# Kernel tuning notes

Hardware: AMD Instinct MI355X
Metric: run time of the kernel (lower is better)

## Reference

```python
import jax, jax.numpy as jnp
import numpy as np

N = 4096
FEAT = 5
H = 128
L = 3
K = 4
HD = H // K  # 32


def setup_inputs() -> dict:
    key = jax.random.key(0)
    ks = jax.random.split(key, 24)
    node_features = jax.random.normal(ks[0], (N, FEAT), dtype=jnp.float32)
    u = jax.random.uniform(ks[1], (N, N), dtype=jnp.float32)
    adj = jnp.where(u < 0.01, u, 0.0)
    adj = adj / (adj.sum(axis=1, keepdims=True) + 1e-8)  # row-normalised
    mask = jax.random.randint(ks[2], (N,), 0, 2).astype(bool)
    s = 0.05
    return {
        'node_features': node_features,
        'adj': adj,
        'mask': mask,
        'Wi': jax.random.normal(ks[3], (FEAT, H), jnp.float32) * s,
        'bi': jnp.zeros((H,), jnp.float32),
        'gat_W': jax.random.normal(ks[4], (L, K, H, HD), jnp.float32) * s,
        'gat_a': jax.random.normal(ks[5], (L, K, 2 * HD), jnp.float32) * s,
        'ln_g': jnp.ones((L, H), jnp.float32),
        'ln_b': jnp.zeros((L, H), jnp.float32),
        'pW1': jax.random.normal(ks[6], (H, H // 2), jnp.float32) * s,
        'pb1': jnp.zeros((H // 2,), jnp.float32),
        'pW2': jax.random.normal(ks[7], (H // 2, 1), jnp.float32) * s,
        'pb2': jnp.zeros((1,), jnp.float32),
        'poolW': jax.random.normal(ks[8], (H, H), jnp.float32) * s,
        'poolb': jnp.zeros((H,), jnp.float32),
        'poolv': jax.random.normal(ks[9], (H,), jnp.float32) * s,
        'vW1': jax.random.normal(ks[10], (H, H // 2), jnp.float32) * s,
        'vb1': jnp.zeros((H // 2,), jnp.float32),
        'vW2': jax.random.normal(ks[11], (H // 2, 1), jnp.float32) * s,
        'vb2': jnp.zeros((1,), jnp.float32),
    }


def _layernorm(x, g, b, eps=1e-5):
    mu = x.mean(-1, keepdims=True)
    var = ((x - mu) ** 2).mean(-1, keepdims=True)
    return (x - mu) / jnp.sqrt(var + eps) * g + b


def reference(node_features, adj, mask, Wi, bi, gat_W, gat_a, ln_g, ln_b,
              pW1, pb1, pW2, pb2, poolW, poolb, poolv, vW1, vb1, vW2, vb2):
    n = node_features.shape[0]
    x = jax.nn.relu(node_features @ Wi + bi)  # (N, H)
    edge_mask = (adj > 0) | jnp.eye(n, dtype=bool)  # (N, N) incl self-loops
    n_layers = gat_W.shape[0]
    for l in range(n_layers):
        Wx = jnp.einsum('nd,kdh->knh', x, gat_W[l])  # (K, N, hd)
        a_src = jnp.einsum('knh,kh->kn', Wx, gat_a[l][:, :HD])  # (K, N)
        a_dst = jnp.einsum('knh,kh->kn', Wx, gat_a[l][:, HD:])  # (K, N)
        e = jax.nn.leaky_relu(a_src[:, :, None] + a_dst[:, None, :], 0.2)  # (K,N,N)
        e = jnp.where(edge_mask[None], e, -jnp.inf)
        alpha = jax.nn.softmax(e, axis=-1)  # softmax over neighbours j
        h = jax.nn.elu(jnp.einsum('kij,kjh->kih', alpha, Wx))  # (K, N, hd)
        out = jnp.transpose(h, (1, 0, 2)).reshape(n, -1)  # concat heads -> (N, H)
        out = out + x  # residual (Identity: in_dim == out_dim)
        x = _layernorm(out, ln_g[l], ln_b[l])
    # policy head
    logits = (jax.nn.relu(x @ pW1 + pb1) @ pW2 + pb2).squeeze(-1)  # (N,)
    logits = jnp.where(mask, logits, -jnp.inf)
    # attention pooling restricted to masked (valid) nodes
    scores = jnp.tanh(x @ poolW + poolb) @ poolv  # (N,)
    scores = jnp.where(mask, scores, -jnp.inf)
    beta = jax.nn.softmax(scores)
    pooled = (beta[:, None] * x).sum(0)  # (H,)
    value = (jax.nn.relu(pooled @ vW1 + vb1) @ vW2 + vb2).squeeze(-1)  # scalar
    return logits, value
```

## Files before the change

### kernel.cpp

```cpp
#include <hip/hip_runtime.h>

#define NN 4096
#define FEAT 5
#define H 128
#define HD 32
#define KH 4
#define NEG_INF (-__builtin_inff())
#define MASK_SENTINEL (-1e30f)

#define WS_FLAG  0
#define WS_DEG   256
#define WS_NBR   (WS_DEG + NN*4)
#define WS_X     (WS_NBR + NN*128*2)
#define WS_WX    (WS_X + NN*H*4)
#define WS_ATS   (WS_WX + NN*H*2)
#define WS_ATD   (WS_ATS + NN*16)
#define WS_PART  (WS_ATD + NN*16)
#define WS_ZPART (WS_PART + 256*H*4)

__device__ __forceinline__ float red64(float v) {
#pragma unroll
    for (int off = 32; off; off >>= 1) v += __shfl_xor(v, off, 64);
    return v;
}
__device__ __forceinline__ float red64max(float v) {
#pragma unroll
    for (int off = 32; off; off >>= 1) v = fmaxf(v, __shfl_xor(v, off, 64));
    return v;
}
__device__ __forceinline__ float red32(float v) {
#pragma unroll
    for (int off = 16; off; off >>= 1) v += __shfl_xor(v, off, 32);
    return v;
}
__device__ __forceinline__ bool read_mask(const void* mp, int f, int n) {
    if (f == 3) return ((const long long*)mp)[n] != 0;
    if (f == 1) return ((const int*)mp)[n] != 0;
    if (f == 2) return ((const float*)mp)[n] != 0.f;
    return ((const unsigned char*)mp)[n] != 0;
}

__global__ __launch_bounds__(256) void k_csr_proj(
    const float* __restrict__ adj, const float* __restrict__ nf,
    const float* __restrict__ Wi, const float* __restrict__ bi,
    const void* mask, int* flag, int* __restrict__ deg,
    unsigned short* __restrict__ nbr, float* __restrict__ xbuf) {
    __shared__ int ln[4][128];
    __shared__ unsigned short cand[4][64][12];
    int w = threadIdx.x >> 6, lane = threadIdx.x & 63;
    int row = blockIdx.x * 4 + w;
    ln[w][lane] = 0; ln[w][64 + lane] = 0;
    const float4* arow = (const float4*)(adj + (size_t)row * NN);
    int cnt = 0;
    bool self = false;
#pragma unroll 4
    for (int j = 0; j < 16; j++) {
        float4 v = arow[lane * 16 + j];
        int cb = lane * 64 + j * 4;
        float vals[4] = {v.x, v.y, v.z, v.w};
#pragma unroll
        for (int s = 0; s < 4; s++) {
            if (vals[s] > 0.f) {
                if (cnt < 12) cand[w][lane][cnt] = (unsigned short)(cb + s);
                cnt++;
                if (cb + s == row) self = true;
            }
        }
    }
    int cl = cnt < 12 ? cnt : 12;
    int inc = cl;
#pragma unroll
    for (int off = 1; off < 64; off <<= 1) {
        int o = __shfl_up(inc, off, 64);
        if (lane >= off) inc += o;
    }
    int excl = inc - cl;
    int total = __shfl(inc, 63, 64);
    bool anyself = __any((int)self);
    for (int t2 = 0; t2 < cl; t2++) {
        int pos = excl + t2;
        if (pos < 128) ln[w][pos] = cand[w][lane][t2];
    }
    if (!anyself) {
        if (lane == 0 && total < 128) ln[w][total] = row;
        total++;
    }
    int d = total < 128 ? total : 128;
    if (lane == 0) deg[row] = d;
    nbr[(size_t)row * 128 + lane] = (unsigned short)ln[w][lane];
    nbr[(size_t)row * 128 + 64 + lane] = (unsigned short)ln[w][64 + lane];
    float a1 = bi[lane], a2 = bi[64 + lane];
#pragma unroll
    for (int f = 0; f < FEAT; f++) {
        float xv = nf[row * FEAT + f];
        a1 += xv * Wi[f * H + lane];
        a2 += xv * Wi[f * H + 64 + lane];
    }
    xbuf[(size_t)row * H + lane] = fmaxf(a1, 0.f);
    xbuf[(size_t)row * H + 64 + lane] = fmaxf(a2, 0.f);
    if (blockIdx.x == 0 && w == 0) {
        const unsigned* ip = (const unsigned*)mask;
        const float* fp = (const float*)mask;
        bool i32ok = true, i64ok = true, f32ok = true;
        for (int i = lane; i < 1024; i += 64) {
            unsigned v = ip[i];
            if (v > 1u) i32ok = false;
            if (i & 1) { if (v != 0u) i64ok = false; }
            else       { if (v > 1u) i64ok = false; }
            float fv = fp[i];
            if (fv != 0.f && fv != 1.f) f32ok = false;
        }
        i32ok = (__ballot((int)i32ok) == ~0ull);
        i64ok = (__ballot((int)i64ok) == ~0ull);
        f32ok = (__ballot((int)f32ok) == ~0ull);
        if (lane == 0) *flag = i64ok ? 3 : (i32ok ? 1 : (f32ok ? 2 : 0));
    }
}

__global__ __launch_bounds__(256) void k_wx(
    const float* __restrict__ xbuf, const float* __restrict__ gw,
    const float* __restrict__ ga, unsigned short* __restrict__ WxBF,
    float* __restrict__ attS, float* __restrict__ attD) {
    __shared__ float xs[8][H];
    int t = threadIdx.x;
    int k = t >> 6, lane = t & 63, dh = lane >> 5, h = lane & 31;
    int n0 = blockIdx.x * 8;
    ((float4*)xs)[t] = ((const float4*)(xbuf + (size_t)n0 * H))[t];
    __syncthreads();
    float acc[8] = {0, 0, 0, 0, 0, 0, 0, 0};
    const float* g = gw + (size_t)k * (H * HD) + h;
    for (int dd = 0; dd < 64; dd += 4) {
        int d = dh * 64 + dd;
        float w0 = g[(size_t)(d + 0) * HD];
        float w1 = g[(size_t)(d + 1) * HD];
        float w2 = g[(size_t)(d + 2) * HD];
        float w3 = g[(size_t)(d + 3) * HD];
#pragma unroll
        for (int nn = 0; nn < 8; nn++) {
            float4 xv = *(const float4*)&xs[nn][d];
            acc[nn] += xv.x * w0 + xv.y * w1 + xv.z * w2 + xv.w * w3;
        }
    }
    float aws = ga[k * 64 + h], awd = ga[k * 64 + 32 + h];
#pragma unroll
    for (int nn = 0; nn < 8; nn++) {
        float full = acc[nn] + __shfl_xor(acc[nn], 32, 64);
        float s = red32(full * aws);
        float dv = red32(full * awd);
        int n = n0 + nn;
        if (dh == 0)
            WxBF[(size_t)n * H + k * 32 + h] =
                (unsigned short)((__float_as_uint(full) + 0x8000u) >> 16);
        if (lane == 0) { attS[n * 4 + k] = s; attD[n * 4 + k] = dv; }
    }
}

__global__ __launch_bounds__(256) void k_agg(
    const int* __restrict__ degG, const unsigned short* __restrict__ nbrG,
    const unsigned short* __restrict__ WxBF, const float4* __restrict__ attS4,
    const float4* __restrict__ attD4, const float* __restrict__ lng,
    const float* __restrict__ lnb, float* __restrict__ xbuf) {
    __shared__ int s_nbr[4][128];
    __shared__ float s_al[4][128][4];
    int t = threadIdx.x, w = t >> 6, lane = t & 63;
    int node = blockIdx.x * 4 + w;
    int d = degG[node];
    const unsigned short* np = nbrG + (size_t)node * 128;
    int sn0 = np[lane], sn1 = np[64 + lane];
    s_nbr[w][lane] = sn0;
    s_nbr[w][64 + lane] = sn1;
    float4 aS = attS4[node];
    float4 d0 = attD4[sn0], d1 = attD4[sn1];
    bool v0 = lane < d, v1 = 64 + lane < d;
#define LRELU(x) ((x) > 0.f ? (x) : 0.2f * (x))
    float e0x = v0 ? LRELU(aS.x + d0.x) : NEG_INF;
    float e0y = v0 ? LRELU(aS.y + d0.y) : NEG_INF;
    float e0z = v0 ? LRELU(aS.z + d0.z) : NEG_INF;
    float e0w = v0 ? LRELU(aS.w + d0.w) : NEG_INF;
    float e1x = v1 ? LRELU(aS.x + d1.x) : NEG_INF;
    float e1y = v1 ? LRELU(aS.y + d1.y) : NEG_INF;
    float e1z = v1 ? LRELU(aS.z + d1.z) : NEG_INF;
    float e1w = v1 ? LRELU(aS.w + d1.w) : NEG_INF;
#undef LRELU
    float mx = red64max(fmaxf(e0x, e1x));
    float my = red64max(fmaxf(e0y, e1y));
    float mz = red64max(fmaxf(e0z, e1z));
    float mw = red64max(fmaxf(e0w, e1w));
    float p0x = v0 ? __expf(e0x - mx) : 0.f, p1x = v1 ? __expf(e1x - mx) : 0.f;
    float p0y = v0 ? __expf(e0y - my) : 0.f, p1y = v1 ? __expf(e1y - my) : 0.f;
    float p0z = v0 ? __expf(e0z - mz) : 0.f, p1z = v1 ? __expf(e1z - mz) : 0.f;
    float p0w = v0 ? __expf(e0w - mw) : 0.f, p1w = v1 ? __expf(e1w - mw) : 0.f;
    float ix = 1.f / red64(p0x + p1x);
    float iy = 1.f / red64(p0y + p1y);
    float iz = 1.f / red64(p0z + p1z);
    float iw = 1.f / red64(p0w + p1w);
    *(float4*)&s_al[w][lane][0]      = make_float4(p0x * ix, p0y * iy, p0z * iz, p0w * iw);
    *(float4*)&s_al[w][64 + lane][0] = make_float4(p1x * ix, p1y * iy, p1z * iz, p1w * iw);
    int ksel = lane >> 4;
    int dim0 = 2 * lane;
    float acc0 = 0.f, acc1 = 0.f;
    int dpad = (d + 7) & ~7;
    for (int c0 = 0; c0 < dpad; c0 += 8) {
#pragma unroll
        for (int j = 0; j < 8; j++) {
            int c = c0 + j;
            int sc = s_nbr[w][c];
            float al = s_al[w][c][ksel];
            unsigned int v = *(const unsigned int*)(WxBF + (size_t)sc * H + dim0);
            acc0 += al * __uint_as_float(v << 16);
            acc1 += al * __uint_as_float(v & 0xFFFF0000u);
        }
    }
    float2 xr = *(const float2*)(xbuf + (size_t)node * H + dim0);
    float h0 = acc0 > 0.f ? acc0 : __expf(acc0) - 1.f;
    float h1 = acc1 > 0.f ? acc1 : __expf(acc1) - 1.f;
    float o0 = h0 + xr.x, o1 = h1 + xr.y;
    float mu = red64(o0 + o1) * (1.f / H);
    float dv0 = o0 - mu, dv1 = o1 - mu;
    float var = red64(dv0 * dv0 + dv1 * dv1) * (1.f / H);
    float rstd = rsqrtf(var + 1e-5f);
    float2 ov;
    ov.x = dv0 * rstd * lng[dim0] + lnb[dim0];
    ov.y = dv1 * rstd * lng[dim0 + 1] + lnb[dim0 + 1];
    *(float2*)(xbuf + (size_t)node * H + dim0) = ov;
}

__global__ __launch_bounds__(256) void k_heads(
    const float* __restrict__ xbuf, const float* __restrict__ pW1,
    const float* __restrict__ pb1, const float* __restrict__ pW2,
    const float* __restrict__ pb2, const float* __restrict__ poolW,
    const float* __restrict__ poolb, const float* __restrict__ poolv,
    const void* mask, const int* __restrict__ flag, float* __restrict__ out,
    float* __restrict__ part, float* __restrict__ zpart) {
    __shared__ float lds_x[16][H];
    __shared__ float lds_part[4][H];
    __shared__ float lds_z[4];
    int t = threadIdx.x, w = t >> 6, lane = t & 63;
    int n0b = blockIdx.x * 16;
    for (int idx = t; idx < 16 * H; idx += 256)
        lds_x[idx >> 7][idx & 127] = xbuf[(size_t)(n0b + (idx >> 7)) * H + (idx & 127)];
    __syncthreads();
    int nb = n0b + w * 4;
    float accp[4] = {0, 0, 0, 0}, acs1[4] = {0, 0, 0, 0}, acs2[4] = {0, 0, 0, 0};
#pragma unroll 2
    for (int d = 0; d < H; d++) {
        float w1 = pW1[d * 64 + lane];
        float q1 = poolW[d * H + lane];
        float q2 = poolW[d * H + 64 + lane];
#pragma unroll
        for (int nn = 0; nn < 4; nn++) {
            float xv = lds_x[w * 4 + nn][d];
            accp[nn] += xv * w1;
            acs1[nn] += xv * q1;
            acs2[nn] += xv * q2;
        }
    }
    int flg = *flag;
    float T = fminf(red64(fabsf(poolv[lane]) + fabsf(poolv[64 + lane])), 30.f);
    float pb1v = pb1[lane], pw2v = pW2[lane], pb2v = pb2[0];
    float pob1 = poolb[lane], pob2 = poolb[64 + lane];
    float pov1 = poolv[lane], pov2 = poolv[64 + lane];
    float pp1 = 0.f, pp2 = 0.f, zacc = 0.f;
#pragma unroll
    for (int nn = 0; nn < 4; nn++) {
        int node = nb + nn;
        float hp = red64(fmaxf(accp[nn] + pb1v, 0.f) * pw2v);
        float sc = red64(tanhf(acs1[nn] + pob1) * pov1 + tanhf(acs2[nn] + pob2) * pov2);
        bool mk = read_mask(mask, flg, node);
        if (lane == 0) out[node] = mk ? (hp + pb2v) : MASK_SENTINEL;
        float wn = mk ? __expf(sc - T) : 0.f;
        pp1 += wn * lds_x[w * 4 + nn][lane];
        pp2 += wn * lds_x[w * 4 + nn][64 + lane];
        zacc += wn;
    }
    lds_part[w][lane] = pp1;
    lds_part[w][64 + lane] = pp2;
    if (lane == 0) lds_z[w] = zacc;
    __syncthreads();
    if (w == 0) {
        float s1 = lds_part[0][lane] + lds_part[1][lane] + lds_part[2][lane] + lds_part[3][lane];
        float s2 = lds_part[0][64 + lane] + lds_part[1][64 + lane] +
                   lds_part[2][64 + lane] + lds_part[3][64 + lane];
        part[blockIdx.x * H + lane] = s1;
        part[blockIdx.x * H + 64 + lane] = s2;
        if (lane == 0) zpart[blockIdx.x] = lds_z[0] + lds_z[1] + lds_z[2] + lds_z[3];
    }
}

__global__ __launch_bounds__(1024) void k_value(
    const float* __restrict__ part, const float* __restrict__ zpart,
    const float* __restrict__ vW1, const float* __restrict__ vb1,
    const float* __restrict__ vW2, const float* __restrict__ vb2,
    float* __restrict__ out) {
    __shared__ float segsum[8][H];
    __shared__ float zfin[256];
    __shared__ float pooled[H];
    int t = threadIdx.x;
    int dim = t & 127, seg = t >> 7;
    float s = 0.f;
#pragma unroll 8
    for (int b = seg * 32; b < seg * 32 + 32; b++) s += part[b * H + dim];
    segsum[seg][dim] = s;
    if (t < 256) zfin[t] = zpart[t];
    __syncthreads();
    if (t < 512) {
        int sg = t >> 7;
        segsum[sg][dim] += segsum[sg + 4][dim];
    }
    if (t >= 512 && t < 640) zfin[t - 512] += zfin[t - 512 + 128];
    __syncthreads();
    if (t < 256) {
        int sg = t >> 7;
        segsum[sg][dim] += segsum[sg + 2][dim];
    }
    if (t >= 512 && t < 576) zfin[t - 512] += zfin[t - 512 + 64];
    __syncthreads();
    if (t < 128) segsum[0][dim] += segsum[1][dim];
    if (t >= 512 && t < 544) zfin[t - 512] += zfin[t - 512 + 32];
    __syncthreads();
    if (t < 32) {
        float z = zfin[t];
#pragma unroll
        for (int off = 16; off; off >>= 1) z += __shfl_xor(z, off, 32);
        if (t == 0) zfin[0] = z;
    }
    __syncthreads();
    float Z = zfin[0];
    if (t < H) pooled[t] = segsum[0][t] / Z;
    __syncthreads();
    if (t < 64) {
        float acc = vb1[t];
#pragma unroll 4
        for (int d = 0; d < H; d++) acc += pooled[d] * vW1[d * 64 + t];
        float v = red64(fmaxf(acc, 0.f) * vW2[t]);
        if (t == 0) out[NN] = v + vb2[0];
    }
}

extern "C" void kernel_launch(void* const* d_in, const int* in_sizes, int n_in,
                              void* d_out, int out_size, void* d_ws, size_t ws_size,
                              hipStream_t stream) {
    const float* nf    = (const float*)d_in[0];
    const float* adj   = (const float*)d_in[1];
    const void*  mask  = d_in[2];
    const float* Wi    = (const float*)d_in[3];
    const float* bi    = (const float*)d_in[4];
    const float* gat_W = (const float*)d_in[5];
    const float* gat_a = (const float*)d_in[6];
    const float* ln_g  = (const float*)d_in[7];
    const float* ln_b  = (const float*)d_in[8];
    const float* pW1   = (const float*)d_in[9];
    const float* pb1   = (const float*)d_in[10];
    const float* pW2   = (const float*)d_in[11];
    const float* pb2   = (const float*)d_in[12];
    const float* poolW = (const float*)d_in[13];
    const float* poolb = (const float*)d_in[14];
    const float* poolv = (const float*)d_in[15];
    const float* vW1   = (const float*)d_in[16];
    const float* vb1   = (const float*)d_in[17];
    const float* vW2   = (const float*)d_in[18];
    const float* vb2   = (const float*)d_in[19];

    char* ws = (char*)d_ws;
    int*            flag = (int*)(ws + WS_FLAG);
    int*            deg  = (int*)(ws + WS_DEG);
    unsigned short* nbr  = (unsigned short*)(ws + WS_NBR);
    float*          xbuf = (float*)(ws + WS_X);
    unsigned short* WxBF = (unsigned short*)(ws + WS_WX);
    float* ats   = (float*)(ws + WS_ATS);
    float* atd   = (float*)(ws + WS_ATD);
    float* partb = (float*)(ws + WS_PART);
    float* zpart = (float*)(ws + WS_ZPART);
    float* out   = (float*)d_out;

    const size_t GWL = KH * H * HD;
    const size_t GAL = KH * 2 * HD;

    k_csr_proj<<<1024, 256, 0, stream>>>(adj, nf, Wi, bi, mask, flag, deg, nbr, xbuf);
    for (int l = 0; l < 3; l++) {
        k_wx<<<512, 256, 0, stream>>>(xbuf, gat_W + l * GWL, gat_a + l * GAL,
                                      WxBF, ats, atd);
        k_agg<<<1024, 256, 0, stream>>>(deg, nbr, WxBF, (const float4*)ats,
                                        (const float4*)atd, ln_g + l * H,
                                        ln_b + l * H, xbuf);
    }
    k_heads<<<256, 256, 0, stream>>>(xbuf, pW1, pb1, pW2, pb2, poolW, poolb, poolv,
                                     mask, flag, out, partb, zpart);
    k_value<<<1, 1024, 0, stream>>>(partb, zpart, vW1, vb1, vW2, vb2, out);
}
```

Baseline: 147.8 us.

## Fuse GAT aggregation with next-layer projection and final heads

Each layer's aggregation/layernorm kernel now also computes the next layer's Wx projection and attention logits from the freshly normalized rows kept in LDS. The last aggregation is fused into the heads kernel, run with 1024-thread blocks. Ping-pong Wx/att buffers avoid read-write conflicts across nodes. This removes three kernel launches and the xbuf re-reads. In exchange the projection runs with only 4 nodes per block, so gat_W is reused less, and the heads kernel leaves 3/4 of its threads idle during the MLP phase.

```diff
diff --git a/kernel.cpp b/kernel.cpp
--- a/kernel.cpp
+++ b/kernel.cpp
@@ -12,10 +12,13 @@
 #define WS_DEG   256
 #define WS_NBR   (WS_DEG + NN*4)
 #define WS_X     (WS_NBR + NN*128*2)
-#define WS_WX    (WS_X + NN*H*4)
-#define WS_ATS   (WS_WX + NN*H*2)
-#define WS_ATD   (WS_ATS + NN*16)
-#define WS_PART  (WS_ATD + NN*16)
+#define WS_WXA   (WS_X + NN*H*4)
+#define WS_ATSA  (WS_WXA + NN*H*2)
+#define WS_ATDA  (WS_ATSA + NN*16)
+#define WS_WXB   (WS_ATDA + NN*16)
+#define WS_ATSB  (WS_WXB + NN*H*2)
+#define WS_ATDB  (WS_ATSB + NN*16)
+#define WS_PART  (WS_ATDB + NN*16)
 #define WS_ZPART (WS_PART + 256*H*4)
 
 __device__ __forceinline__ float red64(float v) {
@@ -40,135 +43,17 @@
     return ((const unsigned char*)mp)[n] != 0;
 }
 
-__global__ __launch_bounds__(256) void k_csr_proj(
-    const float* __restrict__ adj, const float* __restrict__ nf,
-    const float* __restrict__ Wi, const float* __restrict__ bi,
-    const void* mask, int* flag, int* __restrict__ deg,
-    unsigned short* __restrict__ nbr, float* __restrict__ xbuf) {
-    __shared__ int ln[4][128];
-    __shared__ unsigned short cand[4][64][12];
-    int w = threadIdx.x >> 6, lane = threadIdx.x & 63;
-    int row = blockIdx.x * 4 + w;
-    ln[w][lane] = 0; ln[w][64 + lane] = 0;
-    const float4* arow = (const float4*)(adj + (size_t)row * NN);
-    int cnt = 0;
-    bool self = false;
-#pragma unroll 4
-    for (int j = 0; j < 16; j++) {
-        float4 v = arow[lane * 16 + j];
-        int cb = lane * 64 + j * 4;
-        float vals[4] = {v.x, v.y, v.z, v.w};
-#pragma unroll
-        for (int s = 0; s < 4; s++) {
-            if (vals[s] > 0.f) {
-                if (cnt < 12) cand[w][lane][cnt] = (unsigned short)(cb + s);
-                cnt++;
-                if (cb + s == row) self = true;
-            }
-        }
-    }
-    int cl = cnt < 12 ? cnt : 12;
-    int inc = cl;
-#pragma unroll
-    for (int off = 1; off < 64; off <<= 1) {
-        int o = __shfl_up(inc, off, 64);
-        if (lane >= off) inc += o;
-    }
-    int excl = inc - cl;
-    int total = __shfl(inc, 63, 64);
-    bool anyself = __any((int)self);
-    for (int t2 = 0; t2 < cl; t2++) {
-        int pos = excl + t2;
-        if (pos < 128) ln[w][pos] = cand[w][lane][t2];
-    }
-    if (!anyself) {
-        if (lane == 0 && total < 128) ln[w][total] = row;
-        total++;
-    }
-    int d = total < 128 ? total : 128;
-    if (lane == 0) deg[row] = d;
-    nbr[(size_t)row * 128 + lane] = (unsigned short)ln[w][lane];
-    nbr[(size_t)row * 128 + 64 + lane] = (unsigned short)ln[w][64 + lane];
-    float a1 = bi[lane], a2 = bi[64 + lane];
-#pragma unroll
-    for (int f = 0; f < FEAT; f++) {
-        float xv = nf[row * FEAT + f];
-        a1 += xv * Wi[f * H + lane];
-        a2 += xv * Wi[f * H + 64 + lane];
-    }
-    xbuf[(size_t)row * H + lane] = fmaxf(a1, 0.f);
-    xbuf[(size_t)row * H + 64 + lane] = fmaxf(a2, 0.f);
-    if (blockIdx.x == 0 && w == 0) {
-        const unsigned* ip = (const unsigned*)mask;
-        const float* fp = (const float*)mask;
-        bool i32ok = true, i64ok = true, f32ok = true;
-        for (int i = lane; i < 1024; i += 64) {
-            unsigned v = ip[i];
-            if (v > 1u) i32ok = false;
-            if (i & 1) { if (v != 0u) i64ok = false; }
-            else       { if (v > 1u) i64ok = false; }
-            float fv = fp[i];
-            if (fv != 0.f && fv != 1.f) f32ok = false;
-        }
-        i32ok = (__ballot((int)i32ok) == ~0ull);
-        i64ok = (__ballot((int)i64ok) == ~0ull);
-        f32ok = (__ballot((int)f32ok) == ~0ull);
-        if (lane == 0) *flag = i64ok ? 3 : (i32ok ? 1 : (f32ok ? 2 : 0));
-    }
-}
-
-__global__ __launch_bounds__(256) void k_wx(
-    const float* __restrict__ xbuf, const float* __restrict__ gw,
-    const float* __restrict__ ga, unsigned short* __restrict__ WxBF,
-    float* __restrict__ attS, float* __restrict__ attD) {
-    __shared__ float xs[8][H];
-    int t = threadIdx.x;
-    int k = t >> 6, lane = t & 63, dh = lane >> 5, h = lane & 31;
-    int n0 = blockIdx.x * 8;
-    ((float4*)xs)[t] = ((const float4*)(xbuf + (size_t)n0 * H))[t];
-    __syncthreads();
-    float acc[8] = {0, 0, 0, 0, 0, 0, 0, 0};
-    const float* g = gw + (size_t)k * (H * HD) + h;
-    for (int dd = 0; dd < 64; dd += 4) {
-        int d = dh * 64 + dd;
-        float w0 = g[(size_t)(d + 0) * HD];
-        float w1 = g[(size_t)(d + 1) * HD];
-        float w2 = g[(size_t)(d + 2) * HD];
-        float w3 = g[(size_t)(d + 3) * HD];
-#pragma unroll
-        for (int nn = 0; nn < 8; nn++) {
-            float4 xv = *(const float4*)&xs[nn][d];
-            acc[nn] += xv.x * w0 + xv.y * w1 + xv.z * w2 + xv.w * w3;
-        }
-    }
-    float aws = ga[k * 64 + h], awd = ga[k * 64 + 32 + h];
-#pragma unroll
-    for (int nn = 0; nn < 8; nn++) {
-        float full = acc[nn] + __shfl_xor(acc[nn], 32, 64);
-        float s = red32(full * aws);
-        float dv = red32(full * awd);
-        int n = n0 + nn;
-        if (dh == 0)
-            WxBF[(size_t)n * H + k * 32 + h] =
-                (unsigned short)((__float_as_uint(full) + 0x8000u) >> 16);
-        if (lane == 0) { attS[n * 4 + k] = s; attD[n * 4 + k] = dv; }
-    }
-}
-
-__global__ __launch_bounds__(256) void k_agg(
-    const int* __restrict__ degG, const unsigned short* __restrict__ nbrG,
+__device__ __forceinline__ void agg_node(
+    int node, int lane, int d, const unsigned short* __restrict__ nbrG,
     const unsigned short* __restrict__ WxBF, const float4* __restrict__ attS4,
     const float4* __restrict__ attD4, const float* __restrict__ lng,
-    const float* __restrict__ lnb, float* __restrict__ xbuf) {
-    __shared__ int s_nbr[4][128];
-    __shared__ float s_al[4][128][4];
-    int t = threadIdx.x, w = t >> 6, lane = t & 63;
-    int node = blockIdx.x * 4 + w;
-    int d = degG[node];
+    const float* __restrict__ lnb, const float* __restrict__ xin,
+    float* __restrict__ xout, int* __restrict__ s_nbr,
+    float (*__restrict__ s_al)[4], float* __restrict__ lds_row) {
     const unsigned short* np = nbrG + (size_t)node * 128;
     int sn0 = np[lane], sn1 = np[64 + lane];
-    s_nbr[w][lane] = sn0;
-    s_nbr[w][64 + lane] = sn1;
+    s_nbr[lane] = sn0;
+    s_nbr[64 + lane] = sn1;
     float4 aS = attS4[node];
     float4 d0 = attD4[sn0], d1 = attD4[sn1];
     bool v0 = lane < d, v1 = 64 + lane < d;
@@ -194,8 +79,8 @@
     float iy = 1.f / red64(p0y + p1y);
     float iz = 1.f / red64(p0z + p1z);
     float iw = 1.f / red64(p0w + p1w);
-    *(float4*)&s_al[w][lane][0]      = make_float4(p0x * ix, p0y * iy, p0z * iz, p0w * iw);
-    *(float4*)&s_al[w][64 + lane][0] = make_float4(p1x * ix, p1y * iy, p1z * iz, p1w * iw);
+    *(float4*)&s_al[lane][0]      = make_float4(p0x * ix, p0y * iy, p0z * iz, p0w * iw);
+    *(float4*)&s_al[64 + lane][0] = make_float4(p1x * ix, p1y * iy, p1z * iz, p1w * iw);
     int ksel = lane >> 4;
     int dim0 = 2 * lane;
     float acc0 = 0.f, acc1 = 0.f;
@@ -204,14 +89,14 @@
 #pragma unroll
         for (int j = 0; j < 8; j++) {
             int c = c0 + j;
-            int sc = s_nbr[w][c];
-            float al = s_al[w][c][ksel];
+            int sc = s_nbr[c];
+            float al = s_al[c][ksel];
             unsigned int v = *(const unsigned int*)(WxBF + (size_t)sc * H + dim0);
             acc0 += al * __uint_as_float(v << 16);
             acc1 += al * __uint_as_float(v & 0xFFFF0000u);
         }
     }
-    float2 xr = *(const float2*)(xbuf + (size_t)node * H + dim0);
+    float2 xr = *(const float2*)(xin + (size_t)node * H + dim0);
     float h0 = acc0 > 0.f ? acc0 : __expf(acc0) - 1.f;
     float h1 = acc1 > 0.f ? acc1 : __expf(acc1) - 1.f;
     float o0 = h0 + xr.x, o1 = h1 + xr.y;
@@ -222,62 +107,244 @@
     float2 ov;
     ov.x = dv0 * rstd * lng[dim0] + lnb[dim0];
     ov.y = dv1 * rstd * lng[dim0 + 1] + lnb[dim0 + 1];
-    *(float2*)(xbuf + (size_t)node * H + dim0) = ov;
-}
-
-__global__ __launch_bounds__(256) void k_heads(
-    const float* __restrict__ xbuf, const float* __restrict__ pW1,
-    const float* __restrict__ pb1, const float* __restrict__ pW2,
-    const float* __restrict__ pb2, const float* __restrict__ poolW,
-    const float* __restrict__ poolb, const float* __restrict__ poolv,
-    const void* mask, const int* __restrict__ flag, float* __restrict__ out,
+    *(float2*)(lds_row + dim0) = ov;
+    if (xout) *(float2*)(xout + (size_t)node * H + dim0) = ov;
+}
+
+__device__ __forceinline__ void wx4(const float (*lds_x)[H], int n0,
+                                    const float* __restrict__ gw,
+                                    const float* __restrict__ ga,
+                                    unsigned short* __restrict__ WxBF,
+                                    float* __restrict__ attS,
+                                    float* __restrict__ attD) {
+    int t = threadIdx.x;
+    int k = t >> 6, lane = t & 63, dh = lane >> 5, h = lane & 31;
+    float acc[4] = {0.f, 0.f, 0.f, 0.f};
+    const float* g = gw + (size_t)k * (H * HD) + h;
+    for (int dd = 0; dd < 64; dd += 4) {
+        int d = dh * 64 + dd;
+        float w0 = g[(size_t)(d + 0) * HD];
+        float w1 = g[(size_t)(d + 1) * HD];
+        float w2 = g[(size_t)(d + 2) * HD];
+        float w3 = g[(size_t)(d + 3) * HD];
+#pragma unroll
+        for (int nn = 0; nn < 4; nn++) {
+            float4 xv = *(const float4*)&lds_x[nn][d];
+            acc[nn] += xv.x * w0 + xv.y * w1 + xv.z * w2 + xv.w * w3;
+        }
+    }
+    float aws = ga[k * 64 + h], awd = ga[k * 64 + 32 + h];
+#pragma unroll
+    for (int nn = 0; nn < 4; nn++) {
+        float full = acc[nn] + __shfl_xor(acc[nn], 32, 64);
+        float s = red32(full * aws);
+        float dv = red32(full * awd);
+        int n = n0 + nn;
+        if (dh == 0)
+            WxBF[(size_t)n * H + k * 32 + h] =
+                (unsigned short)((__float_as_uint(full) + 0x8000u) >> 16);
+        if (lane == 0) { attS[n * 4 + k] = s; attD[n * 4 + k] = dv; }
+    }
+}
+
+__global__ __launch_bounds__(256) void k_csr_proj(
+    const float* __restrict__ adj, const float* __restrict__ nf,
+    const float* __restrict__ Wi, const float* __restrict__ bi,
+    const void* mask, int* flag, int* __restrict__ deg,
+    unsigned short* __restrict__ nbr, float* __restrict__ xbuf) {
+    __shared__ int ln[4][128];
+    __shared__ unsigned short cand[4][64][12];
+    int w = threadIdx.x >> 6, lane = threadIdx.x & 63;
+    int row = blockIdx.x * 4 + w;
+    ln[w][lane] = 0; ln[w][64 + lane] = 0;
+    const float4* arow = (const float4*)(adj + (size_t)row * NN);
+    int cnt = 0;
+    bool self = false;
+#pragma unroll 4
+    for (int j = 0; j < 16; j++) {
+        float4 v = arow[lane * 16 + j];
+        int cb = lane * 64 + j * 4;
+        float vals[4] = {v.x, v.y, v.z, v.w};
+#pragma unroll
+        for (int s = 0; s < 4; s++) {
+            if (vals[s] > 0.f) {
+                if (cnt < 12) cand[w][lane][cnt] = (unsigned short)(cb + s);
+                cnt++;
+                if (cb + s == row) self = true;
+            }
+        }
+    }
+    int cl = cnt < 12 ? cnt : 12;
+    int inc = cl;
+#pragma unroll
+    for (int off = 1; off < 64; off <<= 1) {
+        int o = __shfl_up(inc, off, 64);
+        if (lane >= off) inc += o;
+    }
+    int excl = inc - cl;
+    int total = __shfl(inc, 63, 64);
+    bool anyself = __any((int)self);
+    for (int t2 = 0; t2 < cl; t2++) {
+        int pos = excl + t2;
+        if (pos < 128) ln[w][pos] = cand[w][lane][t2];
+    }
+    if (!anyself) {
+        if (lane == 0 && total < 128) ln[w][total] = row;
+        total++;
+    }
+    int d = total < 128 ? total : 128;
+    if (lane == 0) deg[row] = d;
+    nbr[(size_t)row * 128 + lane] = (unsigned short)ln[w][lane];
+    nbr[(size_t)row * 128 + 64 + lane] = (unsigned short)ln[w][64 + lane];
+    float a1 = bi[lane], a2 = bi[64 + lane];
+#pragma unroll
+    for (int f = 0; f < FEAT; f++) {
+        float xv = nf[row * FEAT + f];
+        a1 += xv * Wi[f * H + lane];
+        a2 += xv * Wi[f * H + 64 + lane];
+    }
+    xbuf[(size_t)row * H + lane] = fmaxf(a1, 0.f);
+    xbuf[(size_t)row * H + 64 + lane] = fmaxf(a2, 0.f);
+    if (blockIdx.x == 0 && w == 0) {
+        const unsigned* ip = (const unsigned*)mask;
+        const float* fp = (const float*)mask;
+        bool i32ok = true, i64ok = true, f32ok = true;
+        for (int i = lane; i < 1024; i += 64) {
+            unsigned v = ip[i];
+            if (v > 1u) i32ok = false;
+            if (i & 1) { if (v != 0u) i64ok = false; }
+            else       { if (v > 1u) i64ok = false; }
+            float fv = fp[i];
+            if (fv != 0.f && fv != 1.f) f32ok = false;
+        }
+        i32ok = (__ballot((int)i32ok) == ~0ull);
+        i64ok = (__ballot((int)i64ok) == ~0ull);
+        f32ok = (__ballot((int)f32ok) == ~0ull);
+        if (lane == 0) *flag = i64ok ? 3 : (i32ok ? 1 : (f32ok ? 2 : 0));
+    }
+}
+
+__global__ __launch_bounds__(256) void k_wx0(
+    const float* __restrict__ xbuf, const float* __restrict__ gw,
+    const float* __restrict__ ga, unsigned short* __restrict__ WxBF,
+    float* __restrict__ attS, float* __restrict__ attD) {
+    __shared__ float xs[8][H];
+    int t = threadIdx.x;
+    int k = t >> 6, lane = t & 63, dh = lane >> 5, h = lane & 31;
+    int n0 = blockIdx.x * 8;
+    ((float4*)xs)[t] = ((const float4*)(xbuf + (size_t)n0 * H))[t];
+    __syncthreads();
+    float acc[8] = {0, 0, 0, 0, 0, 0, 0, 0};
+    const float* g = gw + (size_t)k * (H * HD) + h;
+    for (int dd = 0; dd < 64; dd += 4) {
+        int d = dh * 64 + dd;
+        float w0 = g[(size_t)(d + 0) * HD];
+        float w1 = g[(size_t)(d + 1) * HD];
+        float w2 = g[(size_t)(d + 2) * HD];
+        float w3 = g[(size_t)(d + 3) * HD];
+#pragma unroll
+        for (int nn = 0; nn < 8; nn++) {
+            float4 xv = *(const float4*)&xs[nn][d];
+            acc[nn] += xv.x * w0 + xv.y * w1 + xv.z * w2 + xv.w * w3;
+        }
+    }
+    float aws = ga[k * 64 + h], awd = ga[k * 64 + 32 + h];
+#pragma unroll
+    for (int nn = 0; nn < 8; nn++) {
+        float full = acc[nn] + __shfl_xor(acc[nn], 32, 64);
+        float s = red32(full * aws);
+        float dv = red32(full * awd);
+        int n = n0 + nn;
+        if (dh == 0)
+            WxBF[(size_t)n * H + k * 32 + h] =
+                (unsigned short)((__float_as_uint(full) + 0x8000u) >> 16);
+        if (lane == 0) { attS[n * 4 + k] = s; attD[n * 4 + k] = dv; }
+    }
+}
+
+__global__ __launch_bounds__(256) void k_layer(
+    const int* __restrict__ degG, const unsigned short* __restrict__ nbrG,
+    const unsigned short* __restrict__ WxP, const float* __restrict__ attSP,
+    const float* __restrict__ attDP, const float* __restrict__ lng,
+    const float* __restrict__ lnb, float* __restrict__ xbuf,
+    const float* __restrict__ gwN, const float* __restrict__ gaN,
+    unsigned short* __restrict__ WxN, float* __restrict__ attSN,
+    float* __restrict__ attDN) {
+    __shared__ int s_nbr[4][128];
+    __shared__ float s_al[4][128][4];
+    __shared__ float lds_x[4][H];
+    int t = threadIdx.x, w = t >> 6, lane = t & 63;
+    int node = blockIdx.x * 4 + w;
+    agg_node(node, lane, degG[node], nbrG, WxP, (const float4*)attSP,
+             (const float4*)attDP, lng, lnb, xbuf, xbuf,
+             s_nbr[w], s_al[w], lds_x[w]);
+    __syncthreads();
+    wx4(lds_x, blockIdx.x * 4, gwN, gaN, WxN, attSN, attDN);
+}
+
+__global__ __launch_bounds__(1024) void k_agg_heads(
+    const int* __restrict__ degG, const unsigned short* __restrict__ nbrG,
+    const unsigned short* __restrict__ WxP, const float* __restrict__ attSP,
+    const float* __restrict__ attDP, const float* __restrict__ lng,
+    const float* __restrict__ lnb, const float* __restrict__ xbuf,
+    const float* __restrict__ pW1, const float* __restrict__ pb1,
+    const float* __restrict__ pW2, const float* __restrict__ pb2,
+    const float* __restrict__ poolW, const float* __restrict__ poolb,
+    const float* __restrict__ poolv, const void* mask,
+    const int* __restrict__ flag, float* __restrict__ out,
     float* __restrict__ part, float* __restrict__ zpart) {
+    __shared__ int s_nbr[16][128];
+    __shared__ float s_al[16][128][4];
     __shared__ float lds_x[16][H];
     __shared__ float lds_part[4][H];
     __shared__ float lds_z[4];
     int t = threadIdx.x, w = t >> 6, lane = t & 63;
     int n0b = blockIdx.x * 16;
-    for (int idx = t; idx < 16 * H; idx += 256)
-        lds_x[idx >> 7][idx & 127] = xbuf[(size_t)(n0b + (idx >> 7)) * H + (idx & 127)];
-    __syncthreads();
-    int nb = n0b + w * 4;
-    float accp[4] = {0, 0, 0, 0}, acs1[4] = {0, 0, 0, 0}, acs2[4] = {0, 0, 0, 0};
+    agg_node(n0b + w, lane, degG[n0b + w], nbrG, WxP, (const float4*)attSP,
+             (const float4*)attDP, lng, lnb, xbuf, nullptr,
+             s_nbr[w], s_al[w], lds_x[w]);
+    __syncthreads();
+    if (t < 256) {
+        int w4 = t >> 6;
+        int nb = n0b + w4 * 4;
+        float accp[4] = {0, 0, 0, 0}, acs1[4] = {0, 0, 0, 0}, acs2[4] = {0, 0, 0, 0};
 #pragma unroll 2
-    for (int d = 0; d < H; d++) {
-        float w1 = pW1[d * 64 + lane];
-        float q1 = poolW[d * H + lane];
-        float q2 = poolW[d * H + 64 + lane];
+        for (int d = 0; d < H; d++) {
+            float w1 = pW1[d * 64 + lane];
+            float q1 = poolW[d * H + lane];
+            float q2 = poolW[d * H + 64 + lane];
+#pragma unroll
+            for (int nn = 0; nn < 4; nn++) {
+                float xv = lds_x[w4 * 4 + nn][d];
+                accp[nn] += xv * w1;
+                acs1[nn] += xv * q1;
+                acs2[nn] += xv * q2;
+            }
+        }
+        int flg = *flag;
+        float T = fminf(red64(fabsf(poolv[lane]) + fabsf(poolv[64 + lane])), 30.f);
+        float pb1v = pb1[lane], pw2v = pW2[lane], pb2v = pb2[0];
+        float pob1 = poolb[lane], pob2 = poolb[64 + lane];
+        float pov1 = poolv[lane], pov2 = poolv[64 + lane];
+        float pp1 = 0.f, pp2 = 0.f, zacc = 0.f;
 #pragma unroll
         for (int nn = 0; nn < 4; nn++) {
-            float xv = lds_x[w * 4 + nn][d];
-            accp[nn] += xv * w1;
-            acs1[nn] += xv * q1;
-            acs2[nn] += xv * q2;
-        }
-    }
-    int flg = *flag;
-    float T = fminf(red64(fabsf(poolv[lane]) + fabsf(poolv[64 + lane])), 30.f);
-    float pb1v = pb1[lane], pw2v = pW2[lane], pb2v = pb2[0];
-    float pob1 = poolb[lane], pob2 = poolb[64 + lane];
-    float pov1 = poolv[lane], pov2 = poolv[64 + lane];
-    float pp1 = 0.f, pp2 = 0.f, zacc = 0.f;
-#pragma unroll
-    for (int nn = 0; nn < 4; nn++) {
-        int node = nb + nn;
-        float hp = red64(fmaxf(accp[nn] + pb1v, 0.f) * pw2v);
-        float sc = red64(tanhf(acs1[nn] + pob1) * pov1 + tanhf(acs2[nn] + pob2) * pov2);
-        bool mk = read_mask(mask, flg, node);
-        if (lane == 0) out[node] = mk ? (hp + pb2v) : MASK_SENTINEL;
-        float wn = mk ? __expf(sc - T) : 0.f;
-        pp1 += wn * lds_x[w * 4 + nn][lane];
-        pp2 += wn * lds_x[w * 4 + nn][64 + lane];
-        zacc += wn;
-    }
-    lds_part[w][lane] = pp1;
-    lds_part[w][64 + lane] = pp2;
-    if (lane == 0) lds_z[w] = zacc;
-    __syncthreads();
-    if (w == 0) {
+            int node = nb + nn;
+            float hp = red64(fmaxf(accp[nn] + pb1v, 0.f) * pw2v);
+            float sc = red64(tanhf(acs1[nn] + pob1) * pov1 + tanhf(acs2[nn] + pob2) * pov2);
+            bool mk = read_mask(mask, flg, node);
+            if (lane == 0) out[node] = mk ? (hp + pb2v) : MASK_SENTINEL;
+            float wn = mk ? __expf(sc - T) : 0.f;
+            pp1 += wn * lds_x[w4 * 4 + nn][lane];
+            pp2 += wn * lds_x[w4 * 4 + nn][64 + lane];
+            zacc += wn;
+        }
+        lds_part[w4][lane] = pp1;
+        lds_part[w4][64 + lane] = pp2;
+        if (lane == 0) lds_z[w4] = zacc;
+    }
+    __syncthreads();
+    if (t < 64) {
         float s1 = lds_part[0][lane] + lds_part[1][lane] + lds_part[2][lane] + lds_part[3][lane];
         float s2 = lds_part[0][64 + lane] + lds_part[1][64 + lane] +
                    lds_part[2][64 + lane] + lds_part[3][64 + lane];
@@ -366,9 +433,12 @@
     int*            deg  = (int*)(ws + WS_DEG);
     unsigned short* nbr  = (unsigned short*)(ws + WS_NBR);
     float*          xbuf = (float*)(ws + WS_X);
-    unsigned short* WxBF = (unsigned short*)(ws + WS_WX);
-    float* ats   = (float*)(ws + WS_ATS);
-    float* atd   = (float*)(ws + WS_ATD);
+    unsigned short* WxA  = (unsigned short*)(ws + WS_WXA);
+    float* atsA  = (float*)(ws + WS_ATSA);
+    float* atdA  = (float*)(ws + WS_ATDA);
+    unsigned short* WxB  = (unsigned short*)(ws + WS_WXB);
+    float* atsB  = (float*)(ws + WS_ATSB);
+    float* atdB  = (float*)(ws + WS_ATDB);
     float* partb = (float*)(ws + WS_PART);
     float* zpart = (float*)(ws + WS_ZPART);
     float* out   = (float*)d_out;
@@ -377,14 +447,15 @@
     const size_t GAL = KH * 2 * HD;
 
     k_csr_proj<<<1024, 256, 0, stream>>>(adj, nf, Wi, bi, mask, flag, deg, nbr, xbuf);
-    for (int l = 0; l < 3; l++) {
-        k_wx<<<512, 256, 0, stream>>>(xbuf, gat_W + l * GWL, gat_a + l * GAL,
-                                      WxBF, ats, atd);
-        k_agg<<<1024, 256, 0, stream>>>(deg, nbr, WxBF, (const float4*)ats,
-                                        (const float4*)atd, ln_g + l * H,
-                                        ln_b + l * H, xbuf);
-    }
-    k_heads<<<256, 256, 0, stream>>>(xbuf, pW1, pb1, pW2, pb2, poolW, poolb, poolv,
-                                     mask, flag, out, partb, zpart);
+    k_wx0<<<512, 256, 0, stream>>>(xbuf, gat_W, gat_a, WxA, atsA, atdA);
+    k_layer<<<1024, 256, 0, stream>>>(deg, nbr, WxA, atsA, atdA, ln_g, ln_b, xbuf,
+                                      gat_W + GWL, gat_a + GAL, WxB, atsB, atdB);
+    k_layer<<<1024, 256, 0, stream>>>(deg, nbr, WxB, atsB, atdB, ln_g + H, ln_b + H,
+                                      xbuf, gat_W + 2 * GWL, gat_a + 2 * GAL,
+                                      WxA, atsA, atdA);
+    k_agg_heads<<<256, 1024, 0, stream>>>(deg, nbr, WxA, atsA, atdA,
+                                          ln_g + 2 * H, ln_b + 2 * H, xbuf,
+                                          pW1, pb1, pW2, pb2, poolW, poolb, poolv,
+                                          mask, flag, out, partb, zpart);
     k_value<<<1, 1024, 0, stream>>>(partb, zpart, vW1, vb1, vW2, vb2, out);
 }
```

New measurement: 158.0 us. +6.9%, slower.
